# Performance work log

Measured on AMD Instinct MI355X. Metric: run time of the kernel, lower is better.

Reference implementation:

```python
import jax, jax.numpy as jnp
import numpy as np

IN_CH, OUT_CH = 64, 128

def _rulebook():
    # Geometric rulebook for a 3x3 stride-2 pad-1 sparse conv on a B x H x W grid.
    rng = np.random.default_rng(0)
    B, H, Wd = 4, 1024, 1024
    N_in = 200000
    Hout = Wout = (H + 2 - 3) // 2 + 1  # 512
    flat = rng.choice(B * H * Wd, size=N_in, replace=False)
    b = flat // (H * Wd)
    rem = flat % (H * Wd)
    y = rem // Wd
    x = rem % Wd
    rules = []
    for k in range(9):
        ky, kx = divmod(k, 3)
        # out*stride - pad + k_off = in  =>  out = (in + pad - k_off) / stride
        ny = y + 1 - ky
        nx = x + 1 - kx
        ok = (ny >= 0) & (nx >= 0) & (ny % 2 == 0) & (nx % 2 == 0)
        oy = ny // 2
        ox = nx // 2
        ok &= (oy < Hout) & (ox < Wout)
        idx = np.nonzero(ok)[0]
        okey = (b[idx] * Hout + oy[idx]) * Wout + ox[idx]
        rules.append((idx, okey))
    all_keys = np.unique(np.concatenate([r[1] for r in rules]))
    n_out = int(all_keys.shape[0])
    R = max(r[0].shape[0] for r in rules)
    in_idx = np.zeros((9, R), np.int32)
    out_idx = np.zeros((9, R), np.int32)
    mask = np.zeros((9, R), bool)
    for k, (idx, okey) in enumerate(rules):
        m = idx.shape[0]
        in_idx[k, :m] = idx
        out_idx[k, :m] = np.searchsorted(all_keys, okey)
        mask[k, :m] = True
    return in_idx, out_idx, mask, n_out, N_in


def setup_inputs() -> dict:
    key = jax.random.key(0)
    k1, k2 = jax.random.split(key)
    in_idx, out_idx, mask, n_out, n_in = _rulebook()
    feats = jax.random.normal(k1, (n_in, IN_CH), jnp.float32)
    W = jax.random.normal(k2, (9, IN_CH, OUT_CH), jnp.float32) * 0.05
    gamma = jnp.ones((OUT_CH,), jnp.float32)
    beta = jnp.zeros((OUT_CH,), jnp.float32)
    return {
        "feats": feats,
        "W": W,
        "gamma": gamma,
        "beta": beta,
        "in_idx": jnp.asarray(in_idx),
        "out_idx": jnp.asarray(out_idx),
        "mask": jnp.asarray(mask),
        "n_out": n_out,
    }


def reference(feats, W, gamma, beta, in_idx, out_idx, mask, n_out):
    # gather: [9, R, Cin]; padded rules are masked to zero so they add nothing
    g = feats[in_idx] * mask[..., None].astype(feats.dtype)
    # GEMM per kernel offset: [9, R, Cout]
    contrib = jnp.einsum("krc,kcd->krd", g, W)
    # scatter-add into dense output feature matrix [N_out, Cout]
    out = jnp.zeros((n_out, W.shape[-1]), feats.dtype).at[out_idx].add(contrib)
    # BatchNorm1d (training mode: biased batch stats over active sites) + ReLU
    mean = out.mean(axis=0)
    var = out.var(axis=0)
    y = gamma * (out - mean) * jax.lax.rsqrt(var + 1e-5) + beta
    return jnp.maximum(y, 0.0)
```

## Files before the change

kernel.cpp:

```cpp
#include <hip/hip_runtime.h>
#include <hip/hip_bf16.h>
#include <stdint.h>

#define IN_CH 64
#define OUT_CH 128

typedef __bf16 bf16x8 __attribute__((ext_vector_type(8)));
typedef float  f32x4  __attribute__((ext_vector_type(4)));

__device__ inline unsigned short f2bf(float f) {
    unsigned u = __float_as_uint(f);
    unsigned r = (u + 0x7fffu + ((u >> 16) & 1u)) >> 16;
    return (unsigned short)r;
}


__global__ void __launch_bounds__(256) prep_kernel(
    int* __restrict__ inv, int invTot, int zero_row, float* __restrict__ sums,
    const float4* __restrict__ f4, ushort* __restrict__ fb, int n4,
    const float* __restrict__ W, ushort* __restrict__ wsw,
    int invBlocks, int cvtBlocks)
{
    const int b = blockIdx.x;
    const int t = threadIdx.x;
    if (b < invBlocks) {
        int i = b * 256 + t;
        if (i < invTot) inv[i] = zero_row;
        if (b == 0) sums[t] = 0.f;
    } else if (b < invBlocks + cvtBlocks) {
        int i = (b - invBlocks) * 256 + t;
        if (i < n4 + 16) {
            ushort4 o;
            if (i < n4) {
                float4 v = f4[i];
                o.x = f2bf(v.x); o.y = f2bf(v.y); o.z = f2bf(v.z); o.w = f2bf(v.w);
            } else {
                o.x = 0; o.y = 0; o.z = 0; o.w = 0;
            }
            ((ushort4*)fb)[i] = o;
        }
    } else {
        int i = (b - invBlocks - cvtBlocks) * 256 + t;
        if (i < 9 * 16 * 64) {
            int lane = i & 63;
            int gh = (i >> 6) & 15;
            int k = i >> 10;
            int half = gh & 1;
            int g = gh >> 1;
            int ch = g * 16 + (lane & 15);
            int in0 = half * 32 + (lane >> 4) * 8;
            ushort v[8];
#pragma unroll
            for (int j = 0; j < 8; ++j)
                v[j] = f2bf(W[((size_t)k * IN_CH + in0 + j) * OUT_CH + ch]);
            *(ushort4*)(wsw + (size_t)i * 8)     = make_ushort4(v[0], v[1], v[2], v[3]);
            *(ushort4*)(wsw + (size_t)i * 8 + 4) = make_ushort4(v[4], v[5], v[6], v[7]);
        }
    }
}

__global__ void __launch_bounds__(256) build_inv_kernel(
    const int* __restrict__ in_idx,
    const int* __restrict__ out_idx,
    const int* __restrict__ mask,
    int* __restrict__ inv,
    int R)
{
    int r = blockIdx.x * 256 + threadIdx.x;
    if (r >= R) return;
    int k = blockIdx.y;
    size_t e = (size_t)k * R + r;
    if (!mask[e]) return;
    inv[(size_t)out_idx[e] * 9 + k] = in_idx[e];
}

__global__ void __launch_bounds__(256, 3) fused_out_kernel(
    const ushort* __restrict__ fb,
    const ushort* __restrict__ wsw,
    const int* __restrict__ inv,
    float* __restrict__ out,
    float* __restrict__ sums,
    int n_out, int zero_row)
{
    const int lane = threadIdx.x & 63;
    const int w = threadIdx.x >> 6;
    const int col = lane & 15;
    const int quad = lane >> 4;
    const int base = blockIdx.x * 128 + w * 32;
    const int eA = base + col;
    const int eB = base + 16 + col;
    const bool okA = eA < n_out;
    const bool okB = eB < n_out;

    int ivA[9], ivB[9];
    {
        const int* __restrict__ pA = inv + (size_t)(okA ? eA : 0) * 9;
        const int* __restrict__ pB = inv + (size_t)(okB ? eB : 0) * 9;
#pragma unroll
        for (int k = 0; k < 9; ++k) ivA[k] = okA ? pA[k] : zero_row;
#pragma unroll
        for (int k = 0; k < 9; ++k) ivB[k] = okB ? pB[k] : zero_row;
    }

    f32x4 accA[8], accB[8];
#pragma unroll
    for (int g = 0; g < 8; ++g) {
        accA[g] = (f32x4){0.f, 0.f, 0.f, 0.f};
        accB[g] = (f32x4){0.f, 0.f, 0.f, 0.f};
    }

    bf16x8 FA0[2], FA1[2], FB0[2], FB1[2];
    {
        const ushort* __restrict__ fa = fb + (size_t)ivA[0] * IN_CH + quad * 8;
        FA0[0] = *(const bf16x8*)fa;
        FA1[0] = *(const bf16x8*)(fa + 32);
        const ushort* __restrict__ fbp = fb + (size_t)ivB[0] * IN_CH + quad * 8;
        FB0[0] = *(const bf16x8*)fbp;
        FB1[0] = *(const bf16x8*)(fbp + 32);
    }

#pragma unroll
    for (int k = 0; k < 9; ++k) {
        const int cur = k & 1;
        const int nxt = cur ^ 1;
        if (k < 8) {
            const ushort* __restrict__ fa = fb + (size_t)ivA[k + 1] * IN_CH + quad * 8;
            FA0[nxt] = *(const bf16x8*)fa;
            FA1[nxt] = *(const bf16x8*)(fa + 32);
            const ushort* __restrict__ fbp = fb + (size_t)ivB[k + 1] * IN_CH + quad * 8;
            FB0[nxt] = *(const bf16x8*)fbp;
            FB1[nxt] = *(const bf16x8*)(fbp + 32);
        }
        const ushort* __restrict__ wk = wsw + (size_t)k * (16 * 64 * 8) + lane * 8;
#pragma unroll
        for (int g = 0; g < 8; ++g) {
            bf16x8 W0 = *(const bf16x8*)(wk + (g * 2 + 0) * 512);
            bf16x8 W1 = *(const bf16x8*)(wk + (g * 2 + 1) * 512);
            accA[g] = __builtin_amdgcn_mfma_f32_16x16x32_bf16(W0, FA0[cur], accA[g], 0, 0, 0);
            accA[g] = __builtin_amdgcn_mfma_f32_16x16x32_bf16(W1, FA1[cur], accA[g], 0, 0, 0);
            accB[g] = __builtin_amdgcn_mfma_f32_16x16x32_bf16(W0, FB0[cur], accB[g], 0, 0, 0);
            accB[g] = __builtin_amdgcn_mfma_f32_16x16x32_bf16(W1, FB1[cur], accB[g], 0, 0, 0);
        }
        __builtin_amdgcn_sched_barrier(0);
    }

    if (okA) {
        float* __restrict__ rp = out + (size_t)eA * OUT_CH + quad * 4;
#pragma unroll
        for (int g = 0; g < 8; ++g)
            *(f32x4*)(rp + g * 16) = accA[g];
    }
    if (okB) {
        float* __restrict__ rp = out + (size_t)eB * OUT_CH + quad * 4;
#pragma unroll
        for (int g = 0; g < 8; ++g)
            *(f32x4*)(rp + g * 16) = accB[g];
    }

    f32x4 ss[8], qq[8];
#pragma unroll
    for (int g = 0; g < 8; ++g) {
        ss[g] = accA[g] + accB[g];
        qq[g] = accA[g] * accA[g] + accB[g] * accB[g];
    }
#pragma unroll
    for (int m = 1; m <= 8; m <<= 1) {
#pragma unroll
        for (int g = 0; g < 8; ++g) {
#pragma unroll
            for (int j = 0; j < 4; ++j) {
                ss[g][j] += __shfl_xor(ss[g][j], m);
                qq[g][j] += __shfl_xor(qq[g][j], m);
            }
        }
    }

    __shared__ float redS[4][OUT_CH];
    __shared__ float redQ[4][OUT_CH];
    if (col == 0) {
#pragma unroll
        for (int g = 0; g < 8; ++g)
#pragma unroll
            for (int j = 0; j < 4; ++j) {
                redS[w][g * 16 + quad * 4 + j] = ss[g][j];
                redQ[w][g * 16 + quad * 4 + j] = qq[g][j];
            }
    }
    __syncthreads();
    if (threadIdx.x < OUT_CH) {
        int c = threadIdx.x;
        float a  = redS[0][c] + redS[1][c] + redS[2][c] + redS[3][c];
        float bq = redQ[0][c] + redQ[1][c] + redQ[2][c] + redQ[3][c];
        atomicAdd(&sums[c], a);
        atomicAdd(&sums[OUT_CH + c], bq);
    }
}

__global__ void __launch_bounds__(256) bn_relu_kernel(
    float4* __restrict__ out,
    const float* __restrict__ sums,
    const float* __restrict__ gamma,
    const float* __restrict__ beta,
    int total4, float inv_n)
{
    int idx = blockIdx.x * 256 + threadIdx.x;
    if (idx >= total4) return;
    int c0 = (idx & 31) * 4;
    float4 v = out[idx];
    float r[4] = {v.x, v.y, v.z, v.w};
#pragma unroll
    for (int j = 0; j < 4; ++j) {
        int c = c0 + j;
        float mean = sums[c] * inv_n;
        float var = sums[OUT_CH + c] * inv_n - mean * mean;
        float scale = gamma[c] * rsqrtf(var + 1e-5f);
        float y = (r[j] - mean) * scale + beta[c];
        r[j] = fmaxf(y, 0.0f);
    }
    out[idx] = make_float4(r[0], r[1], r[2], r[3]);
}


__global__ void __launch_bounds__(256) zero_kernel(float4* __restrict__ out, int n4,
                                                   float* __restrict__ sums) {
    int idx = blockIdx.x * 256 + threadIdx.x;
    if (idx < n4) out[idx] = make_float4(0.f, 0.f, 0.f, 0.f);
    if (blockIdx.x == 0 && threadIdx.x < 2 * OUT_CH) sums[threadIdx.x] = 0.f;
}

__global__ void __launch_bounds__(256) scatter_gemm_kernel(
    const float* __restrict__ feats,
    const float* __restrict__ W,
    const int* __restrict__ in_idx,
    const int* __restrict__ out_idx,
    const int* __restrict__ mask,
    float* __restrict__ acc,
    int R)
{
    const int lane = threadIdx.x & 63;
    const int waveId = threadIdx.x >> 6;
    const int half = waveId & 1;
    const int pair = waveId >> 1;
    const int k = blockIdx.y;
    const int c = half * 64 + lane;

    float wreg[IN_CH];
    const float* __restrict__ wp = W + (size_t)k * IN_CH * OUT_CH + c;
#pragma unroll
    for (int i = 0; i < IN_CH; ++i) wreg[i] = wp[i * OUT_CH];

    const int r0 = blockIdx.x * 128;
    const int rEnd = min(r0 + 128, R);
    const int* __restrict__ maskK = mask + (size_t)k * R;
    const int* __restrict__ inK = in_idx + (size_t)k * R;
    const int* __restrict__ outK = out_idx + (size_t)k * R;

    for (int r = r0 + pair; r < rEnd; r += 2) {
        if (!__builtin_amdgcn_readfirstlane(maskK[r])) continue;
        int in = __builtin_amdgcn_readfirstlane(inK[r]);
        int out = __builtin_amdgcn_readfirstlane(outK[r]);
        const float* __restrict__ f = feats + (size_t)in * IN_CH;
        float s = 0.f, s1 = 0.f;
#pragma unroll
        for (int i = 0; i < IN_CH; i += 2) {
            s = fmaf(wreg[i], f[i], s);
            s1 = fmaf(wreg[i + 1], f[i + 1], s1);
        }
        atomicAdd(acc + (size_t)out * OUT_CH + c, s + s1);
    }
}

__global__ void __launch_bounds__(128) stats_kernel(
    const float* __restrict__ acc,
    float* __restrict__ sums,
    int n_out)
{
    int c = threadIdx.x;
    float s = 0.0f, s2 = 0.0f;
    for (int r = blockIdx.x; r < n_out; r += gridDim.x) {
        float v = acc[(size_t)r * OUT_CH + c];
        s += v;
        s2 += v * v;
    }
    atomicAdd(&sums[c], s);
    atomicAdd(&sums[OUT_CH + c], s2);
}


extern "C" void kernel_launch(void* const* d_in, const int* in_sizes, int n_in,
                              void* d_out, int out_size, void* d_ws, size_t ws_size,
                              hipStream_t stream) {
    const float* feats   = (const float*)d_in[0];
    const float* W       = (const float*)d_in[1];
    const float* gamma   = (const float*)d_in[2];
    const float* beta    = (const float*)d_in[3];
    const int*   in_idx  = (const int*)d_in[4];
    const int*   out_idx = (const int*)d_in[5];
    const int*   mask    = (const int*)d_in[6];

    const int R = in_sizes[4] / 9;
    const int n_out = out_size / OUT_CH;
    const int N_in = in_sizes[0] / IN_CH;
    float* acc = (float*)d_out;

    size_t off_inv  = 0;
    size_t sz_inv   = (size_t)n_out * 9 * sizeof(int);
    size_t off_sums = (off_inv + sz_inv + 15) & ~(size_t)15;
    size_t off_fb   = (off_sums + 1024 + 15) & ~(size_t)15;
    size_t off_wsw  = (off_fb + (size_t)(N_in + 1) * IN_CH * 2 + 15) & ~(size_t)15;
    size_t needed   = off_wsw + (size_t)9 * OUT_CH * IN_CH * 2;

    if (ws_size >= needed) {
        int*    inv  = (int*)((char*)d_ws + off_inv);
        float*  sums = (float*)((char*)d_ws + off_sums);
        ushort* fb   = (ushort*)((char*)d_ws + off_fb);
        ushort* wsw  = (ushort*)((char*)d_ws + off_wsw);

        const int invTot = n_out * 9;
        const int n4 = N_in * IN_CH / 4;
        const int invBlocks = (invTot + 255) / 256;
        const int cvtBlocks = (n4 + 16 + 255) / 256;
        const int wswBlocks = (9 * 16 * 64 + 255) / 256;

        prep_kernel<<<invBlocks + cvtBlocks + wswBlocks, 256, 0, stream>>>(
            inv, invTot, N_in, sums,
            (const float4*)feats, fb, n4,
            W, wsw, invBlocks, cvtBlocks);

        dim3 gridB((R + 255) / 256, 9);
        build_inv_kernel<<<gridB, 256, 0, stream>>>(in_idx, out_idx, mask, inv, R);

        fused_out_kernel<<<(n_out + 127) / 128, 256, 0, stream>>>(
            fb, wsw, inv, acc, sums, n_out, N_in);

        int total4 = out_size / 4;
        bn_relu_kernel<<<(total4 + 255) / 256, 256, 0, stream>>>(
            (float4*)acc, sums, gamma, beta, total4, 1.0f / (float)n_out);
    } else {
        float* sums = (float*)d_ws;
        int n4 = out_size / 4;
        zero_kernel<<<(n4 + 255) / 256, 256, 0, stream>>>((float4*)acc, n4, sums);

        dim3 grid((R + 127) / 128, 9);
        scatter_gemm_kernel<<<grid, 256, 0, stream>>>(feats, W, in_idx, out_idx, mask, acc, R);

        stats_kernel<<<2048, 128, 0, stream>>>(acc, sums, n_out);

        int total4 = out_size / 4;
        bn_relu_kernel<<<(total4 + 255) / 256, 256, 0, stream>>>(
            (float4*)acc, sums, gamma, beta, total4, 1.0f / (float)n_out);
    }
}
```

Before: 433.3 us.

## Stage per-offset weights in LDS via async global_load_lds with deeper feature prefetch

Weight tiles for each kernel offset are now copied into double-buffered LDS with async global-to-LDS loads shared by all four waves, instead of every wave reading weights from global memory. Feature gathers are prefetched two offsets ahead with a triple buffer, and explicit vmcnt waits plus block barriers order the pipeline. Occupancy hint is raised from 3 to 4 blocks per CU. The change adds 32KB of LDS and a block barrier per offset, and the hand-counted vmcnt values must match the exact number of outstanding loads.

```diff
diff --git a/kernel.cpp b/kernel.cpp
--- a/kernel.cpp
+++ b/kernel.cpp
@@ -12,6 +12,12 @@
     unsigned u = __float_as_uint(f);
     unsigned r = (u + 0x7fffu + ((u >> 16) & 1u)) >> 16;
     return (unsigned short)r;
+}
+
+__device__ inline void gload_lds16(const void* g, void* l) {
+    __builtin_amdgcn_global_load_lds(
+        (const __attribute__((address_space(1))) unsigned int*)g,
+        (__attribute__((address_space(3))) unsigned int*)l, 16, 0, 0);
 }
 
 
@@ -74,7 +80,7 @@
     inv[(size_t)out_idx[e] * 9 + k] = in_idx[e];
 }
 
-__global__ void __launch_bounds__(256, 3) fused_out_kernel(
+__global__ void __launch_bounds__(256, 4) fused_out_kernel(
     const ushort* __restrict__ fb,
     const ushort* __restrict__ wsw,
     const int* __restrict__ inv,
@@ -82,6 +88,11 @@
     float* __restrict__ sums,
     int n_out, int zero_row)
 {
+    __shared__ __align__(16) char smraw[32768];
+    ushort (* __restrict__ ldsW)[8192] = (ushort(*)[8192])smraw;
+    float* redS = (float*)smraw;
+    float* redQ = (float*)(smraw + 2048);
+
     const int lane = threadIdx.x & 63;
     const int w = threadIdx.x >> 6;
     const int col = lane & 15;
@@ -101,6 +112,11 @@
 #pragma unroll
         for (int k = 0; k < 9; ++k) ivB[k] = okB ? pB[k] : zero_row;
     }
+    asm volatile("s_waitcnt vmcnt(0)" ::: "memory");
+    __builtin_amdgcn_sched_barrier(0);
+
+    const int sWave = w * 4096;
+    const int sLane = sWave + lane * 16;
 
     f32x4 accA[8], accB[8];
 #pragma unroll
@@ -109,39 +125,73 @@
         accB[g] = (f32x4){0.f, 0.f, 0.f, 0.f};
     }
 
-    bf16x8 FA0[2], FA1[2], FB0[2], FB1[2];
+    bf16x8 FA0[3], FA1[3], FB0[3], FB1[3];
+
     {
-        const ushort* __restrict__ fa = fb + (size_t)ivA[0] * IN_CH + quad * 8;
-        FA0[0] = *(const bf16x8*)fa;
-        FA1[0] = *(const bf16x8*)(fa + 32);
-        const ushort* __restrict__ fbp = fb + (size_t)ivB[0] * IN_CH + quad * 8;
-        FB0[0] = *(const bf16x8*)fbp;
-        FB1[0] = *(const bf16x8*)(fbp + 32);
+#pragma unroll
+        for (int j = 0; j < 4; ++j)
+            gload_lds16((const char*)wsw + sLane + j * 1024,
+                        smraw + sWave + j * 1024);
+        __builtin_amdgcn_sched_barrier(0);
+#pragma unroll
+        for (int d = 0; d < 2; ++d) {
+            const ushort* fa = fb + (size_t)ivA[d] * IN_CH + quad * 8;
+            FA0[d] = *(const bf16x8*)fa;
+            FA1[d] = *(const bf16x8*)(fa + 32);
+            const ushort* fbp = fb + (size_t)ivB[d] * IN_CH + quad * 8;
+            FB0[d] = *(const bf16x8*)fbp;
+            FB1[d] = *(const bf16x8*)(fbp + 32);
+            __builtin_amdgcn_sched_barrier(0);
+        }
+        asm volatile("s_waitcnt vmcnt(8)" ::: "memory");
+        __builtin_amdgcn_s_barrier();
+        __builtin_amdgcn_sched_barrier(0);
     }
 
 #pragma unroll
     for (int k = 0; k < 9; ++k) {
         const int cur = k & 1;
         const int nxt = cur ^ 1;
+        const int fcur = k % 3;
+        const int f2 = (k + 2) % 3;
+
         if (k < 8) {
-            const ushort* __restrict__ fa = fb + (size_t)ivA[k + 1] * IN_CH + quad * 8;
-            FA0[nxt] = *(const bf16x8*)fa;
-            FA1[nxt] = *(const bf16x8*)(fa + 32);
-            const ushort* __restrict__ fbp = fb + (size_t)ivB[k + 1] * IN_CH + quad * 8;
-            FB0[nxt] = *(const bf16x8*)fbp;
-            FB1[nxt] = *(const bf16x8*)(fbp + 32);
-        }
-        const ushort* __restrict__ wk = wsw + (size_t)k * (16 * 64 * 8) + lane * 8;
+#pragma unroll
+            for (int j = 0; j < 4; ++j)
+                gload_lds16((const char*)wsw + (size_t)(k + 1) * 16384 + sLane + j * 1024,
+                            smraw + nxt * 16384 + sWave + j * 1024);
+            __builtin_amdgcn_sched_barrier(0);
+        }
+        if (k < 7) {
+            const ushort* fa = fb + (size_t)ivA[k + 2] * IN_CH + quad * 8;
+            FA0[f2] = *(const bf16x8*)fa;
+            FA1[f2] = *(const bf16x8*)(fa + 32);
+            const ushort* fbp = fb + (size_t)ivB[k + 2] * IN_CH + quad * 8;
+            FB0[f2] = *(const bf16x8*)fbp;
+            FB1[f2] = *(const bf16x8*)(fbp + 32);
+            __builtin_amdgcn_sched_barrier(0);
+        }
+
+        const ushort* wl = &ldsW[cur][lane * 8];
 #pragma unroll
         for (int g = 0; g < 8; ++g) {
-            bf16x8 W0 = *(const bf16x8*)(wk + (g * 2 + 0) * 512);
-            bf16x8 W1 = *(const bf16x8*)(wk + (g * 2 + 1) * 512);
-            accA[g] = __builtin_amdgcn_mfma_f32_16x16x32_bf16(W0, FA0[cur], accA[g], 0, 0, 0);
-            accA[g] = __builtin_amdgcn_mfma_f32_16x16x32_bf16(W1, FA1[cur], accA[g], 0, 0, 0);
-            accB[g] = __builtin_amdgcn_mfma_f32_16x16x32_bf16(W0, FB0[cur], accB[g], 0, 0, 0);
-            accB[g] = __builtin_amdgcn_mfma_f32_16x16x32_bf16(W1, FB1[cur], accB[g], 0, 0, 0);
-        }
-        __builtin_amdgcn_sched_barrier(0);
+            bf16x8 W0 = *(const bf16x8*)(wl + (g * 2 + 0) * 512);
+            bf16x8 W1 = *(const bf16x8*)(wl + (g * 2 + 1) * 512);
+            accA[g] = __builtin_amdgcn_mfma_f32_16x16x32_bf16(W0, FA0[fcur], accA[g], 0, 0, 0);
+            accA[g] = __builtin_amdgcn_mfma_f32_16x16x32_bf16(W1, FA1[fcur], accA[g], 0, 0, 0);
+            accB[g] = __builtin_amdgcn_mfma_f32_16x16x32_bf16(W0, FB0[fcur], accB[g], 0, 0, 0);
+            accB[g] = __builtin_amdgcn_mfma_f32_16x16x32_bf16(W1, FB1[fcur], accB[g], 0, 0, 0);
+        }
+
+        if (k < 7) {
+            asm volatile("s_waitcnt vmcnt(4)" ::: "memory");
+            __builtin_amdgcn_s_barrier();
+            __builtin_amdgcn_sched_barrier(0);
+        } else if (k == 7) {
+            asm volatile("s_waitcnt vmcnt(0)" ::: "memory");
+            __builtin_amdgcn_s_barrier();
+            __builtin_amdgcn_sched_barrier(0);
+        }
     }
 
     if (okA) {
@@ -175,22 +225,21 @@
         }
     }
 
-    __shared__ float redS[4][OUT_CH];
-    __shared__ float redQ[4][OUT_CH];
+    __syncthreads();
     if (col == 0) {
 #pragma unroll
         for (int g = 0; g < 8; ++g)
 #pragma unroll
             for (int j = 0; j < 4; ++j) {
-                redS[w][g * 16 + quad * 4 + j] = ss[g][j];
-                redQ[w][g * 16 + quad * 4 + j] = qq[g][j];
+                redS[w * OUT_CH + g * 16 + quad * 4 + j] = ss[g][j];
+                redQ[w * OUT_CH + g * 16 + quad * 4 + j] = qq[g][j];
             }
     }
     __syncthreads();
     if (threadIdx.x < OUT_CH) {
         int c = threadIdx.x;
-        float a  = redS[0][c] + redS[1][c] + redS[2][c] + redS[3][c];
-        float bq = redQ[0][c] + redQ[1][c] + redQ[2][c] + redQ[3][c];
+        float a  = redS[c] + redS[OUT_CH + c] + redS[2 * OUT_CH + c] + redS[3 * OUT_CH + c];
+        float bq = redQ[c] + redQ[OUT_CH + c] + redQ[2 * OUT_CH + c] + redQ[3 * OUT_CH + c];
         atomicAdd(&sums[c], a);
         atomicAdd(&sums[OUT_CH + c], bq);
     }
```

Result: slower. 458.5 us (+5.8%).
